# Kernel optimization log

Hardware: AMD Instinct MI355X
Metric: run time of the kernel (lower is better)

## Reference

```python
import jax, jax.numpy as jnp
import numpy as np

DIM = 256
HEADS = 8
HEAD_DIM = DIM // HEADS
EDGE_TYPES = 8  # edge_type_count; table has EDGE_TYPES+1 rows, row 0 is padding
B, N = 2, 2048
EPS = 1e-5


def layer_norm(x, g, b):
    mu = jnp.mean(x, axis=-1, keepdims=True)
    var = jnp.mean(jnp.square(x - mu), axis=-1, keepdims=True)
    return (x - mu) * jax.lax.rsqrt(var + EPS) * g + b


def setup_inputs() -> dict:
    key = jax.random.key(0)
    ks = jax.random.split(key, 12)
    s = 0.02
    x = jax.random.normal(ks[0], (B, N, DIM), dtype=jnp.float32)
    edge_types = jax.random.randint(ks[1], (B, N, N), 0, EDGE_TYPES + 1, dtype=jnp.int32)
    node_mask = jax.random.randint(ks[2], (B, N), 0, 2, dtype=jnp.int32).astype(bool)
    qkv_w = jax.random.normal(ks[3], (DIM, 3 * DIM), dtype=jnp.float32) * s
    qkv_b = jnp.zeros((3 * DIM,), jnp.float32)
    proj_w = jax.random.normal(ks[4], (DIM, DIM), dtype=jnp.float32) * s
    proj_b = jnp.zeros((DIM,), jnp.float32)
    edge_bias_table = jax.random.normal(ks[5], (EDGE_TYPES + 1, HEADS), dtype=jnp.float32) * s
    edge_bias_table = edge_bias_table.at[0].set(0.0)  # padding_idx=0
    ln1_g = jnp.ones((DIM,), jnp.float32); ln1_b = jnp.zeros((DIM,), jnp.float32)
    ln2_g = jnp.ones((DIM,), jnp.float32); ln2_b = jnp.zeros((DIM,), jnp.float32)
    ffn_w1 = jax.random.normal(ks[6], (DIM, 4 * DIM), dtype=jnp.float32) * s
    ffn_b1 = jnp.zeros((4 * DIM,), jnp.float32)
    ffn_w2 = jax.random.normal(ks[7], (4 * DIM, DIM), dtype=jnp.float32) * s
    ffn_b2 = jnp.zeros((DIM,), jnp.float32)
    return dict(x=x, edge_types=edge_types, node_mask=node_mask,
                qkv_w=qkv_w, qkv_b=qkv_b, proj_w=proj_w, proj_b=proj_b,
                edge_bias_table=edge_bias_table, ln1_g=ln1_g, ln1_b=ln1_b,
                ln2_g=ln2_g, ln2_b=ln2_b, ffn_w1=ffn_w1, ffn_b1=ffn_b1,
                ffn_w2=ffn_w2, ffn_b2=ffn_b2)


def reference(x, edge_types, node_mask, qkv_w, qkv_b, proj_w, proj_b,
              edge_bias_table, ln1_g, ln1_b, ln2_g, ln2_b,
              ffn_w1, ffn_b1, ffn_w2, ffn_b2):
    scale = HEAD_DIM ** -0.5
    residual = x
    h = layer_norm(x, ln1_g, ln1_b)
    qkv = h @ qkv_w + qkv_b                         # [B,N,3*DIM]
    qkv = qkv.reshape(B, N, 3, HEADS, HEAD_DIM)
    q, k, v = (qkv[:, :, 0].transpose(0, 2, 1, 3),  # [B,H,N,d]
               qkv[:, :, 1].transpose(0, 2, 1, 3),
               qkv[:, :, 2].transpose(0, 2, 1, 3))
    scores = jnp.einsum('bhnd,bhmd->bhnm', q, k) * scale
    bias = edge_bias_table[edge_types]              # [B,N,N,H]
    scores = scores + bias.transpose(0, 3, 1, 2)    # [B,H,N,N]
    eye = jnp.eye(N, dtype=bool)
    edge_mask = (edge_types != 0) | eye[None]
    node_mask_2d = node_mask[:, None, :] & node_mask[:, :, None]
    attn_mask = edge_mask & node_mask_2d            # [B,N,N]
    scores = jnp.where(attn_mask[:, None], scores, -1e9)
    attn = jax.nn.softmax(scores, axis=-1)
    out = jnp.einsum('bhnm,bhmd->bhnd', attn, v)
    out = out.transpose(0, 2, 1, 3).reshape(B, N, DIM)
    out = (out @ proj_w + proj_b) * node_mask[:, :, None]
    x1 = residual + out
    h2 = layer_norm(x1, ln2_g, ln2_b)
    h2 = jax.nn.gelu(h2 @ ffn_w1 + ffn_b1, approximate=False) @ ffn_w2 + ffn_b2
    h2 = h2 * node_mask[:, :, None]
    return x1 + h2
```

## Files before the change

### kernel.cpp

```cpp
#include <hip/hip_runtime.h>
#include <math.h>

#define DIMM 256
#define HEADS 8
#define NB 2048
#define BB 2
#define ROWS (BB*NB)

typedef __attribute__((ext_vector_type(8))) short bf16x8;
typedef __attribute__((ext_vector_type(4))) float f32x4;

__device__ inline unsigned short f2bf(float f) {
    unsigned int u = __float_as_uint(f);
    u += 0x7FFFu + ((u >> 16) & 1u);
    return (unsigned short)(u >> 16);
}
__device__ inline float bf2f(unsigned short u) {
    return __uint_as_float(((unsigned int)u) << 16);
}

__device__ inline int get_mask(const void* nm, int fmt, int idx) {
    if (fmt) return ((const unsigned char*)nm)[idx] != 0;
    return ((const int*)nm)[idx] != 0;
}

__device__ inline void ln8_body(const float* __restrict__ x, const float* __restrict__ g,
                                const float* __restrict__ bb, unsigned short* __restrict__ o,
                                int row, int lane32) {
    int c0 = lane32 * 8;
    float4 v0 = *(const float4*)&x[(size_t)row * DIMM + c0];
    float4 v1 = *(const float4*)&x[(size_t)row * DIMM + c0 + 4];
    float s  = v0.x + v0.y + v0.z + v0.w + v1.x + v1.y + v1.z + v1.w;
    float s2 = v0.x*v0.x + v0.y*v0.y + v0.z*v0.z + v0.w*v0.w
             + v1.x*v1.x + v1.y*v1.y + v1.z*v1.z + v1.w*v1.w;
#pragma unroll
    for (int off = 16; off >= 1; off >>= 1) {
        s  += __shfl_xor(s,  off);
        s2 += __shfl_xor(s2, off);
    }
    float mean = s * (1.0f / DIMM);
    float var  = s2 * (1.0f / DIMM) - mean * mean;
    float rstd = rsqrtf(var + 1e-5f);
    float4 g0 = *(const float4*)&g[c0],  g1 = *(const float4*)&g[c0 + 4];
    float4 b0 = *(const float4*)&bb[c0], b1 = *(const float4*)&bb[c0 + 4];
    ushort4 u0, u1;
    u0.x = f2bf((v0.x - mean) * rstd * g0.x + b0.x);
    u0.y = f2bf((v0.y - mean) * rstd * g0.y + b0.y);
    u0.z = f2bf((v0.z - mean) * rstd * g0.z + b0.z);
    u0.w = f2bf((v0.w - mean) * rstd * g0.w + b0.w);
    u1.x = f2bf((v1.x - mean) * rstd * g1.x + b1.x);
    u1.y = f2bf((v1.y - mean) * rstd * g1.y + b1.y);
    u1.z = f2bf((v1.z - mean) * rstd * g1.z + b1.z);
    u1.w = f2bf((v1.w - mean) * rstd * g1.w + b1.w);
    *(ushort4*)&o[(size_t)row * DIMM + c0]     = u0;
    *(ushort4*)&o[(size_t)row * DIMM + c0 + 4] = u1;
}

__global__ __launch_bounds__(256) void prep_kernel(
    const float* __restrict__ w0, const float* __restrict__ w1,
    const float* __restrict__ w2, const float* __restrict__ w3,
    unsigned short* __restrict__ o0, unsigned short* __restrict__ o1,
    unsigned short* __restrict__ o2, unsigned short* __restrict__ o3,
    const float* __restrict__ x, const float* __restrict__ ln1_g,
    const float* __restrict__ ln1_b, unsigned short* __restrict__ h_ln,
    const int* __restrict__ etypes, const void* __restrict__ nmask,
    unsigned char* __restrict__ emaskP)
{
    __shared__ float tile[64][65];
    __shared__ int fsh;
    int bid = blockIdx.x, t = threadIdx.x;
    if (bid < 192) {
        const float* src; unsigned short* dst; int K, N, idx;
        if (bid < 48)       { src = w0; dst = o0; K = 256;  N = 768;  idx = bid; }
        else if (bid < 64)  { src = w1; dst = o1; K = 256;  N = 256;  idx = bid - 48; }
        else if (bid < 128) { src = w2; dst = o2; K = 256;  N = 1024; idx = bid - 64; }
        else                { src = w3; dst = o3; K = 1024; N = 256;  idx = bid - 128; }
        int ntiles = N >> 6;
        int k0 = (idx / ntiles) * 64, n0 = (idx % ntiles) * 64;
        int r = t >> 4, c4 = (t & 15) * 4;
#pragma unroll
        for (int i = 0; i < 4; ++i) {
            float4 v = *(const float4*)&src[(size_t)(k0 + r + i * 16) * N + n0 + c4];
            tile[r + i * 16][c4 + 0] = v.x;
            tile[r + i * 16][c4 + 1] = v.y;
            tile[r + i * 16][c4 + 2] = v.z;
            tile[r + i * 16][c4 + 3] = v.w;
        }
        __syncthreads();
#pragma unroll
        for (int i = 0; i < 4; ++i) {
            int n = n0 + r + i * 16;
            ushort4 u;
            u.x = f2bf(tile[c4 + 0][r + i * 16]);
            u.y = f2bf(tile[c4 + 1][r + i * 16]);
            u.z = f2bf(tile[c4 + 2][r + i * 16]);
            u.w = f2bf(tile[c4 + 3][r + i * 16]);
            *(ushort4*)&dst[(size_t)n * K + k0 + c4] = u;
        }
    } else if (bid < 704) {
        int row = (bid - 192) * 8 + (t >> 5);
        ln8_body(x, ln1_g, ln1_b, h_ln, row, t & 31);
    } else {
        if (t == 0) fsh = 0;
        __syncthreads();
        if (((const unsigned char*)nmask)[4 * t + 1] != 0) fsh = 1;
        __syncthreads();
        int fm = fsh;
        int unit = (bid - 704) * 4 + (t >> 6);
        int lane = t & 63, quad = lane >> 4, l15 = lane & 15;
        int b = unit >> 12;
        int qt16 = (unit >> 5) & 127;
        int kt = unit & 31;
        int dw[4];
#pragma unroll
        for (int r = 0; r < 4; ++r) {
            int qr = qt16 * 16 + quad * 4 + r;
            int rowv = get_mask(nmask, fm, b * NB + qr);
            unsigned int pk = 0u;
#pragma unroll
            for (int ct = 0; ct < 4; ++ct) {
                int col = kt * 64 + ct * 16 + l15;
                int et = etypes[(size_t)(b * NB + qr) * NB + col];
                int colv = get_mask(nmask, fm, b * NB + col);
                int valid = rowv && colv && ((et != 0) || (col == qr));
                pk |= (valid ? (unsigned int)(et + 1) : 0u) << (ct * 8);
            }
            dw[r] = (int)pk;
        }
        int4 o = {dw[0], dw[1], dw[2], dw[3]};
        *(int4*)(emaskP + (size_t)unit * 1024 + lane * 16) = o;
    }
}

__global__ __launch_bounds__(256) void gemm_qkv_mfma(
    const unsigned short* __restrict__ A, const unsigned short* __restrict__ Bt,
    const float* __restrict__ bias,
    unsigned short* __restrict__ qkvh, unsigned short* __restrict__ vT)
{
    const int K = 256;
    int t = threadIdx.x, w = t >> 6, l = t & 63;
    int l15 = l & 15, quad = l >> 4;
    int n0 = blockIdx.x * 64;
    int m0 = blockIdx.y * 64;
    const unsigned short* ap = A + (size_t)(m0 + w * 16 + l15) * K + quad * 8;
    const unsigned short* bp = Bt + (size_t)(n0 + l15) * K + quad * 8;

    f32x4 acc[4];
#pragma unroll
    for (int c = 0; c < 4; ++c) acc[c] = (f32x4){0.f, 0.f, 0.f, 0.f};

    bf16x8 aA, bA[4], aB, bB[4];
    auto ld = [&](bf16x8& af, bf16x8 (&bf)[4], int k0) {
        af = *(const bf16x8*)(ap + k0);
#pragma unroll
        for (int c = 0; c < 4; ++c)
            bf[c] = *(const bf16x8*)(bp + (size_t)(c * 16) * K + k0);
    };
    auto pr = [&](const bf16x8& af, const bf16x8 (&bf)[4]) {
#pragma unroll
        for (int c = 0; c < 4; ++c)
            acc[c] = __builtin_amdgcn_mfma_f32_16x16x32_bf16(af, bf[c], acc[c], 0, 0, 0);
    };
    ld(aA, bA, 0);
    for (int k0 = 0; k0 < K; k0 += 64) {
        ld(aB, bB, k0 + 32);
        pr(aA, bA);
        if (k0 + 64 < K) ld(aA, bA, k0 + 64);
        pr(aB, bB);
    }

    if (n0 < 512) {
#pragma unroll
        for (int r = 0; r < 4; ++r) {
            int row = m0 + w * 16 + quad * 4 + r;
#pragma unroll
            for (int c = 0; c < 4; ++c) {
                int col = n0 + c * 16 + l15;
                qkvh[(size_t)row * 512 + col] = f2bf(acc[c][r] + bias[col]);
            }
        }
    } else {
        int bb_ = m0 >> 11;
        int n = (m0 + w * 16 + quad * 4) & 2047;
#pragma unroll
        for (int c = 0; c < 4; ++c) {
            int col = n0 + c * 16 + l15 - 512;
            int hidx = col >> 5, d = col & 31;
            float bs = bias[n0 + c * 16 + l15];
            ushort4 u;
            u.x = f2bf(acc[c][0] + bs);
            u.y = f2bf(acc[c][1] + bs);
            u.z = f2bf(acc[c][2] + bs);
            u.w = f2bf(acc[c][3] + bs);
            *(ushort4*)&vT[(size_t)((bb_ * HEADS + hidx) * 32 + d) * NB + n] = u;
        }
    }
}

__global__ __launch_bounds__(256) void attn_mfma(
    const unsigned short* __restrict__ qkvh,
    const unsigned short* __restrict__ vT,
    const unsigned char* __restrict__ emaskP,
    const float* __restrict__ table,
    unsigned short* __restrict__ OpH, float* __restrict__ lpart)
{
    __shared__ unsigned short P[4][16][72];
    __shared__ float tab2m[16];

    int t = threadIdx.x;
    int w = t >> 6, l = t & 63;
    int l15 = l & 15, quad = l >> 4;
    int h = blockIdx.y;
    int z = blockIdx.z, b = z >> 2, sp = z & 3;
    int q0 = blockIdx.x * 64 + w * 16;
    int kbase = sp * (NB / 4);

    if (t < 16) tab2m[t] = (t >= 1 && t < 10) ? __expf(table[(t - 1) * 8 + h]) : 0.f;
    __syncthreads();

    const float scale = 0.17677669529663689f;

    bf16x8 aq = *(const bf16x8*)(qkvh + (size_t)(b * NB + q0 + l15) * 512 + h * 32 + quad * 8);

    const unsigned short* kp = qkvh + (size_t)(b * NB + l15) * 512 + 256 + h * 32 + quad * 8;
    const unsigned short* vp = vT + (size_t)((b * HEADS + h) * 32 + l15) * NB + quad * 8;
    int qt16 = blockIdx.x * 4 + w;
    const unsigned char* ep = emaskP + (size_t)((b * 128 + qt16) * 32) * 1024 + l * 16;

    float lacc[4] = {0.f, 0.f, 0.f, 0.f};
    f32x4 O0 = {0.f, 0.f, 0.f, 0.f}, O1 = {0.f, 0.f, 0.f, 0.f};

    auto loadtile = [&](bf16x8 (&kf)[4], bf16x8 (&vf)[2][2], int4& ef, int m0) {
#pragma unroll
        for (int ct = 0; ct < 4; ++ct)
            kf[ct] = *(const bf16x8*)(kp + (size_t)(m0 + ct * 16) * 512);
#pragma unroll
        for (int ks = 0; ks < 2; ++ks) {
            vf[ks][0] = *(const bf16x8*)(vp + m0 + ks * 32);
            vf[ks][1] = *(const bf16x8*)(vp + 16 * NB + m0 + ks * 32);
        }
        ef = *(const int4*)(ep + (size_t)(m0 >> 6) * 1024);
    };

    auto process = [&](const bf16x8 (&kf)[4], const bf16x8 (&vf)[2][2], const int4& ef) {
        unsigned int ew[4] = {(unsigned int)ef.x, (unsigned int)ef.y,
                              (unsigned int)ef.z, (unsigned int)ef.w};
#pragma unroll
        for (int ct = 0; ct < 4; ++ct) {
            f32x4 zero = {0.f, 0.f, 0.f, 0.f};
            f32x4 s = __builtin_amdgcn_mfma_f32_16x16x32_bf16(aq, kf[ct], zero, 0, 0, 0);
#pragma unroll
            for (int r = 0; r < 4; ++r) {
                unsigned int c = (ew[r] >> (ct * 8)) & 0xffu;
                float p = __expf(s[r] * scale) * tab2m[c];
                lacc[r] += p;
                P[w][quad * 4 + r][ct * 16 + l15] = f2bf(p);
            }
        }
#pragma unroll
        for (int ks = 0; ks < 2; ++ks) {
            bf16x8 pa = *(const bf16x8*)&P[w][l15][ks * 32 + quad * 8];
            O0 = __builtin_amdgcn_mfma_f32_16x16x32_bf16(pa, vf[ks][0], O0, 0, 0, 0);
            O1 = __builtin_amdgcn_mfma_f32_16x16x32_bf16(pa, vf[ks][1], O1, 0, 0, 0);
        }
    };

    bf16x8 kA[4], kB[4];
    bf16x8 vA[2][2], vB[2][2];
    int4 eA, eB;

    loadtile(kA, vA, eA, kbase);
    for (int m0 = kbase; m0 < kbase + NB / 4; m0 += 128) {
        loadtile(kB, vB, eB, m0 + 64);
        process(kA, vA, eA);
        if (m0 + 128 < kbase + NB / 4) loadtile(kA, vA, eA, m0 + 128);
        process(kB, vB, eB);
    }

    unsigned short* Ob = OpH + (size_t)sp * ROWS * DIMM;
#pragma unroll
    for (int r = 0; r < 4; ++r) {
        float s = lacc[r];
        s += __shfl_xor(s, 1); s += __shfl_xor(s, 2);
        s += __shfl_xor(s, 4); s += __shfl_xor(s, 8);
        int row = b * NB + q0 + quad * 4 + r;
        Ob[(size_t)row * DIMM + h * 32 + l15]      = f2bf(O0[r]);
        Ob[(size_t)row * DIMM + h * 32 + 16 + l15] = f2bf(O1[r]);
        if (l15 == 0) lpart[(size_t)sp * ROWS * 8 + (size_t)row * 8 + h] = s;
    }
}

__global__ __launch_bounds__(1024) void megaback(
    const unsigned short* __restrict__ OpH, const float* __restrict__ lpart,
    const unsigned short* __restrict__ projT, const float* __restrict__ proj_b,
    const float* __restrict__ x, const void* __restrict__ nmask,
    const float* __restrict__ g2, const float* __restrict__ b2,
    const unsigned short* __restrict__ f1T, const float* __restrict__ ffn_b1,
    const unsigned short* __restrict__ f2T, const float* __restrict__ ffn_b2,
    float* __restrict__ out)
{
    __shared__ float rinv_l[16][8];
    __shared__ float stats[16][2];
    __shared__ float redn[16][16][2];
    __shared__ unsigned short Astage[16][264];
    __shared__ float x1s[16][260];
    __shared__ unsigned short hstage[16][264];
    __shared__ unsigned short midstage[16][1032];
    __shared__ int fsh;

    int t = threadIdx.x;
    int w = t >> 6, l = t & 63;
    int l15 = l & 15, quad = l >> 4;
    int grow0 = blockIdx.x * 16;

    if (t == 0) fsh = 0;
    __syncthreads();
    if (((const unsigned char*)nmask)[4 * t + 1] != 0) fsh = 1;

    if (t < 128) {
        int row = t >> 3, h = t & 7;
        float s = 0.f;
#pragma unroll
        for (int sp = 0; sp < 4; ++sp)
            s += lpart[(size_t)sp * ROWS * 8 + (size_t)(grow0 + row) * 8 + h];
        rinv_l[row][h] = (s > 0.f) ? 1.f / s : 0.f;
    }
    __syncthreads();
    int fm = fsh;

    {
        int row = t >> 6, col4 = (t & 63) * 4;
        float rinv = rinv_l[row][col4 >> 5];
        float o0 = 0.f, o1 = 0.f, o2 = 0.f, o3 = 0.f;
#pragma unroll
        for (int sp = 0; sp < 4; ++sp) {
            ushort4 u = *(const ushort4*)&OpH[(size_t)sp * ROWS * DIMM +
                                             (size_t)(grow0 + row) * DIMM + col4];
            o0 += bf2f(u.x); o1 += bf2f(u.y); o2 += bf2f(u.z); o3 += bf2f(u.w);
        }
        ushort4 u;
        u.x = f2bf(o0 * rinv); u.y = f2bf(o1 * rinv);
        u.z = f2bf(o2 * rinv); u.w = f2bf(o3 * rinv);
        *(ushort4*)&Astage[row][col4] = u;
    }
    __syncthreads();

    {
        int col = w * 16 + l15;
        f32x4 acc = (f32x4){0.f, 0.f, 0.f, 0.f};
        const unsigned short* bp = projT + (size_t)col * 256 + quad * 8;
        bf16x8 sb[4];
#pragma unroll
        for (int i = 0; i < 4; ++i) sb[i] = *(const bf16x8*)(bp + i * 32);
#pragma unroll
        for (int ch = 0; ch < 8; ++ch) {
            bf16x8 a = *(const bf16x8*)&Astage[l15][ch * 32 + quad * 8];
            acc = __builtin_amdgcn_mfma_f32_16x16x32_bf16(a, sb[ch & 3], acc, 0, 0, 0);
            if (ch + 4 < 8) sb[ch & 3] = *(const bf16x8*)(bp + (ch + 4) * 32);
        }
        float bs = proj_b[col];
#pragma unroll
        for (int r = 0; r < 4; ++r) {
            int row = quad * 4 + r, grow = grow0 + row;
            float mk = (float)get_mask(nmask, fm, grow);
            float v = (acc[r] + bs) * mk + x[(size_t)grow * DIMM + col];
            x1s[row][col] = v;
            float s = v, s2 = v * v;
#pragma unroll
            for (int off = 1; off < 16; off <<= 1) {
                s += __shfl_xor(s, off); s2 += __shfl_xor(s2, off);
            }
            if (l15 == 0) { redn[row][w][0] = s; redn[row][w][1] = s2; }
        }
    }
    __syncthreads();
    if (t < 16) {
        float s = 0.f, s2 = 0.f;
#pragma unroll
        for (int ww = 0; ww < 16; ++ww) { s += redn[t][ww][0]; s2 += redn[t][ww][1]; }
        float mean = s * (1.f / DIMM);
        float var  = s2 * (1.f / DIMM) - mean * mean;
        stats[t][0] = mean; stats[t][1] = rsqrtf(var + 1e-5f);
    }
    __syncthreads();

    {
        int col = w * 16 + l15;
        float gv = g2[col], bv = b2[col];
#pragma unroll
        for (int r = 0; r < 4; ++r) {
            int row = quad * 4 + r;
            float hv = (x1s[row][col] - stats[row][0]) * stats[row][1] * gv + bv;
            hstage[row][col] = f2bf(hv);
        }
    }
    __syncthreads();

    {
        f32x4 acc[4];
#pragma unroll
        for (int c = 0; c < 4; ++c) acc[c] = (f32x4){0.f, 0.f, 0.f, 0.f};
        const unsigned short* bp = f1T + (size_t)(w * 64 + l15) * 256 + quad * 8;
        bf16x8 bA[4], bB[4];
#pragma unroll
        for (int c = 0; c < 4; ++c) bA[c] = *(const bf16x8*)(bp + (size_t)(c * 16) * 256);
#pragma unroll
        for (int ch = 0; ch < 8; ++ch) {
            bf16x8 a = *(const bf16x8*)&hstage[l15][ch * 32 + quad * 8];
            if (ch + 1 < 8) {
#pragma unroll
                for (int c = 0; c < 4; ++c)
                    bB[c] = *(const bf16x8*)(bp + (size_t)(c * 16) * 256 + (ch + 1) * 32);
            }
#pragma unroll
            for (int c = 0; c < 4; ++c)
                acc[c] = __builtin_amdgcn_mfma_f32_16x16x32_bf16(a, bA[c], acc[c], 0, 0, 0);
#pragma unroll
            for (int c = 0; c < 4; ++c) bA[c] = bB[c];
        }
#pragma unroll
        for (int c = 0; c < 4; ++c) {
            int col = w * 64 + c * 16 + l15;
            float bs = ffn_b1[col];
#pragma unroll
            for (int r = 0; r < 4; ++r) {
                float v = acc[c][r] + bs;
                float x2 = v * v;
                float p = v * fmaf(0.07135481f, x2, 1.5957691f);
                float e = __expf(p);
                float gl = v * (e / (e + 1.f));
                midstage[quad * 4 + r][col] = f2bf(gl);
            }
        }
    }
    __syncthreads();

    {
        int col = w * 16 + l15;
        f32x4 acc = (f32x4){0.f, 0.f, 0.f, 0.f};
        const unsigned short* bp = f2T + (size_t)col * 1024 + quad * 8;
        bf16x8 sb[4];
#pragma unroll
        for (int i = 0; i < 4; ++i) sb[i] = *(const bf16x8*)(bp + i * 32);
#pragma unroll
        for (int ch = 0; ch < 32; ++ch) {
            bf16x8 a = *(const bf16x8*)&midstage[l15][ch * 32 + quad * 8];
            acc = __builtin_amdgcn_mfma_f32_16x16x32_bf16(a, sb[ch & 3], acc, 0, 0, 0);
            if (ch + 4 < 32) sb[ch & 3] = *(const bf16x8*)(bp + (ch + 4) * 32);
        }
        float bs = ffn_b2[col];
#pragma unroll
        for (int r = 0; r < 4; ++r) {
            int row = quad * 4 + r, grow = grow0 + row;
            float mk = (float)get_mask(nmask, fm, grow);
            out[(size_t)grow * DIMM + col] = x1s[row][col] + (acc[r] + bs) * mk;
        }
    }
}

extern "C" void kernel_launch(void* const* d_in, const int* in_sizes, int n_in,
                              void* d_out, int out_size, void* d_ws, size_t ws_size,
                              hipStream_t stream) {
    const float* x       = (const float*)d_in[0];
    const int*   etypes  = (const int*)d_in[1];
    const void*  nmask   = d_in[2];
    const float* qkv_w   = (const float*)d_in[3];
    const float* qkv_b   = (const float*)d_in[4];
    const float* proj_w  = (const float*)d_in[5];
    const float* proj_b  = (const float*)d_in[6];
    const float* table   = (const float*)d_in[7];
    const float* ln1_g   = (const float*)d_in[8];
    const float* ln1_b   = (const float*)d_in[9];
    const float* ln2_g   = (const float*)d_in[10];
    const float* ln2_b   = (const float*)d_in[11];
    const float* ffn_w1  = (const float*)d_in[12];
    const float* ffn_b1  = (const float*)d_in[13];
    const float* ffn_w2  = (const float*)d_in[14];
    const float* ffn_b2  = (const float*)d_in[15];
    float* out = (float*)d_out;
    float* ws  = (float*)d_ws;

    float* lpart = ws;
    unsigned short* ub = (unsigned short*)(ws + 131072);
    unsigned short* h_ln   = ub;
    unsigned short* qkvh   = ub + 1048576;
    unsigned short* vT     = ub + 3145728;
    unsigned short* OpH    = ub + 4194304;
    unsigned short* qkvT   = ub + 8388608;
    unsigned short* projT  = ub + 8585216;
    unsigned short* f1T    = ub + 8650752;
    unsigned short* f2T    = ub + 8912896;
    unsigned char* emaskP  = (unsigned char*)(ub + 9175040);

    prep_kernel<<<dim3(2752), dim3(256), 0, stream>>>(
        qkv_w, proj_w, ffn_w1, ffn_w2, qkvT, projT, f1T, f2T,
        x, ln1_g, ln1_b, h_ln, etypes, nmask, emaskP);
    gemm_qkv_mfma<<<dim3(12, 64), dim3(256), 0, stream>>>(h_ln, qkvT, qkv_b, qkvh, vT);
    attn_mfma<<<dim3(NB/64, HEADS, BB*4), dim3(256), 0, stream>>>(
        qkvh, vT, emaskP, table, OpH, lpart);
    megaback<<<dim3(ROWS/16), dim3(1024), 0, stream>>>(
        OpH, lpart, projT, proj_b, x, nmask, ln2_g, ln2_b,
        f1T, ffn_b1, f2T, ffn_b2, out);
}
```

Measured before the change: 233.1 us.

## Compute transposed attention scores so P feeds PV MFMA from registers

The attention kernel now computes S^T = K·Q^T, so each lane holds four consecutive key columns for one query row. The probabilities can then be packed straight into a bf16x4 operand for the 16x16x16 MFMA against V, with no LDS round trip through the shared P buffer. The softmax scale is folded into Q in the QKV GEMM epilogue. The edge-mask packing kernel is rearranged to match the new column order and now uses vectorized int4 loads of edge types and node masks. The trade-off is more MFMA instructions of a smaller shape, plus bf16 rounding of Q after scaling.

```diff
diff --git a/kernel.cpp b/kernel.cpp
--- a/kernel.cpp
+++ b/kernel.cpp
@@ -8,6 +8,7 @@
 #define ROWS (BB*NB)
 
 typedef __attribute__((ext_vector_type(8))) short bf16x8;
+typedef __attribute__((ext_vector_type(4))) short bf16x4;
 typedef __attribute__((ext_vector_type(4))) float f32x4;
 
 __device__ inline unsigned short f2bf(float f) {
@@ -111,21 +112,32 @@
         int b = unit >> 12;
         int qt16 = (unit >> 5) & 127;
         int kt = unit & 31;
+        int qr = qt16 * 16 + l15;
+        int rowv = get_mask(nmask, fm, b * NB + qr);
+        const int* erow = etypes + (size_t)(b * NB + qr) * NB;
         int dw[4];
 #pragma unroll
-        for (int r = 0; r < 4; ++r) {
-            int qr = qt16 * 16 + quad * 4 + r;
-            int rowv = get_mask(nmask, fm, b * NB + qr);
+        for (int t16 = 0; t16 < 4; ++t16) {
+            int col0 = kt * 64 + t16 * 16 + quad * 4;
+            int4 e4 = *(const int4*)(erow + col0);
+            int ee[4] = {e4.x, e4.y, e4.z, e4.w};
+            int cv[4];
+            if (fm) {
+                unsigned int m4 = *(const unsigned int*)((const unsigned char*)nmask + b * NB + col0);
+                cv[0] = (m4 & 0xffu) != 0;     cv[1] = (m4 & 0xff00u) != 0;
+                cv[2] = (m4 & 0xff0000u) != 0; cv[3] = (m4 >> 24) != 0;
+            } else {
+                int4 m4 = *(const int4*)((const int*)nmask + b * NB + col0);
+                cv[0] = m4.x != 0; cv[1] = m4.y != 0; cv[2] = m4.z != 0; cv[3] = m4.w != 0;
+            }
             unsigned int pk = 0u;
 #pragma unroll
-            for (int ct = 0; ct < 4; ++ct) {
-                int col = kt * 64 + ct * 16 + l15;
-                int et = etypes[(size_t)(b * NB + qr) * NB + col];
-                int colv = get_mask(nmask, fm, b * NB + col);
-                int valid = rowv && colv && ((et != 0) || (col == qr));
-                pk |= (valid ? (unsigned int)(et + 1) : 0u) << (ct * 8);
+            for (int r = 0; r < 4; ++r) {
+                int col = col0 + r;
+                int valid = rowv && cv[r] && ((ee[r] != 0) || (col == qr));
+                pk |= (valid ? (unsigned int)(ee[r] + 1) : 0u) << (r * 8);
             }
-            dw[r] = (int)pk;
+            dw[t16] = (int)pk;
         }
         int4 o = {dw[0], dw[1], dw[2], dw[3]};
         *(int4*)(emaskP + (size_t)unit * 1024 + lane * 16) = o;
@@ -170,13 +182,14 @@
     }
 
     if (n0 < 512) {
+        float sc = (n0 < 256) ? 0.17677669529663689f : 1.0f;
 #pragma unroll
         for (int r = 0; r < 4; ++r) {
             int row = m0 + w * 16 + quad * 4 + r;
 #pragma unroll
             for (int c = 0; c < 4; ++c) {
                 int col = n0 + c * 16 + l15;
-                qkvh[(size_t)row * 512 + col] = f2bf(acc[c][r] + bias[col]);
+                qkvh[(size_t)row * 512 + col] = f2bf((acc[c][r] + bias[col]) * sc);
             }
         }
     } else {
@@ -204,7 +217,6 @@
     const float* __restrict__ table,
     unsigned short* __restrict__ OpH, float* __restrict__ lpart)
 {
-    __shared__ unsigned short P[4][16][72];
     __shared__ float tab2m[16];
 
     int t = threadIdx.x;
@@ -213,81 +225,75 @@
     int h = blockIdx.y;
     int z = blockIdx.z, b = z >> 2, sp = z & 3;
     int q0 = blockIdx.x * 64 + w * 16;
-    int kbase = sp * (NB / 4);
+    int kbase = sp * (NB / 4), kend = kbase + NB / 4;
 
     if (t < 16) tab2m[t] = (t >= 1 && t < 10) ? __expf(table[(t - 1) * 8 + h]) : 0.f;
     __syncthreads();
 
-    const float scale = 0.17677669529663689f;
-
-    bf16x8 aq = *(const bf16x8*)(qkvh + (size_t)(b * NB + q0 + l15) * 512 + h * 32 + quad * 8);
-
-    const unsigned short* kp = qkvh + (size_t)(b * NB + l15) * 512 + 256 + h * 32 + quad * 8;
-    const unsigned short* vp = vT + (size_t)((b * HEADS + h) * 32 + l15) * NB + quad * 8;
+    bf16x8 bq = *(const bf16x8*)(qkvh + (size_t)(b * NB + q0 + l15) * 512 + h * 32 + quad * 8);
+
+    const unsigned short* kp  = qkvh + (size_t)(b * NB + l15) * 512 + 256 + h * 32 + quad * 8;
+    const unsigned short* vp0 = vT + (size_t)((b * HEADS + h) * 32 + l15) * NB + quad * 4;
+    const unsigned short* vp1 = vp0 + (size_t)16 * NB;
     int qt16 = blockIdx.x * 4 + w;
     const unsigned char* ep = emaskP + (size_t)((b * 128 + qt16) * 32) * 1024 + l * 16;
 
-    float lacc[4] = {0.f, 0.f, 0.f, 0.f};
+    float lacc = 0.f;
     f32x4 O0 = {0.f, 0.f, 0.f, 0.f}, O1 = {0.f, 0.f, 0.f, 0.f};
 
-    auto loadtile = [&](bf16x8 (&kf)[4], bf16x8 (&vf)[2][2], int4& ef, int m0) {
-#pragma unroll
-        for (int ct = 0; ct < 4; ++ct)
-            kf[ct] = *(const bf16x8*)(kp + (size_t)(m0 + ct * 16) * 512);
-#pragma unroll
-        for (int ks = 0; ks < 2; ++ks) {
-            vf[ks][0] = *(const bf16x8*)(vp + m0 + ks * 32);
-            vf[ks][1] = *(const bf16x8*)(vp + 16 * NB + m0 + ks * 32);
+    bf16x8 kA[4], kB[4];
+    bf16x4 vA[4][2], vB[4][2];
+    int4 eA, eB;
+
+    auto loadtile = [&](bf16x8 (&kf)[4], bf16x4 (&vf)[4][2], int4& ef, int m0) {
+#pragma unroll
+        for (int t16 = 0; t16 < 4; ++t16) {
+            kf[t16]    = *(const bf16x8*)(kp + (size_t)(m0 + t16 * 16) * 512);
+            vf[t16][0] = *(const bf16x4*)(vp0 + m0 + t16 * 16);
+            vf[t16][1] = *(const bf16x4*)(vp1 + m0 + t16 * 16);
         }
         ef = *(const int4*)(ep + (size_t)(m0 >> 6) * 1024);
     };
 
-    auto process = [&](const bf16x8 (&kf)[4], const bf16x8 (&vf)[2][2], const int4& ef) {
-        unsigned int ew[4] = {(unsigned int)ef.x, (unsigned int)ef.y,
-                              (unsigned int)ef.z, (unsigned int)ef.w};
-#pragma unroll
-        for (int ct = 0; ct < 4; ++ct) {
+    auto process = [&](const bf16x8 (&kf)[4], const bf16x4 (&vf)[4][2], const int4& ef) {
+        int ew[4] = {ef.x, ef.y, ef.z, ef.w};
+#pragma unroll
+        for (int t16 = 0; t16 < 4; ++t16) {
             f32x4 zero = {0.f, 0.f, 0.f, 0.f};
-            f32x4 s = __builtin_amdgcn_mfma_f32_16x16x32_bf16(aq, kf[ct], zero, 0, 0, 0);
-#pragma unroll
-            for (int r = 0; r < 4; ++r) {
-                unsigned int c = (ew[r] >> (ct * 8)) & 0xffu;
-                float p = __expf(s[r] * scale) * tab2m[c];
-                lacc[r] += p;
-                P[w][quad * 4 + r][ct * 16 + l15] = f2bf(p);
-            }
-        }
-#pragma unroll
-        for (int ks = 0; ks < 2; ++ks) {
-            bf16x8 pa = *(const bf16x8*)&P[w][l15][ks * 32 + quad * 8];
-            O0 = __builtin_amdgcn_mfma_f32_16x16x32_bf16(pa, vf[ks][0], O0, 0, 0, 0);
-            O1 = __builtin_amdgcn_mfma_f32_16x16x32_bf16(pa, vf[ks][1], O1, 0, 0, 0);
+            f32x4 sT = __builtin_amdgcn_mfma_f32_16x16x32_bf16(kf[t16], bq, zero, 0, 0, 0);
+            unsigned int e = (unsigned int)ew[t16];
+            float p0 = __expf(sT[0]) * tab2m[e & 0xffu];
+            float p1 = __expf(sT[1]) * tab2m[(e >> 8) & 0xffu];
+            float p2 = __expf(sT[2]) * tab2m[(e >> 16) & 0xffu];
+            float p3 = __expf(sT[3]) * tab2m[e >> 24];
+            lacc += (p0 + p1) + (p2 + p3);
+            bf16x4 pb;
+            pb[0] = (short)f2bf(p0); pb[1] = (short)f2bf(p1);
+            pb[2] = (short)f2bf(p2); pb[3] = (short)f2bf(p3);
+            O0 = __builtin_amdgcn_mfma_f32_16x16x16bf16_1k(vf[t16][0], pb, O0, 0, 0, 0);
+            O1 = __builtin_amdgcn_mfma_f32_16x16x16bf16_1k(vf[t16][1], pb, O1, 0, 0, 0);
         }
     };
 
-    bf16x8 kA[4], kB[4];
-    bf16x8 vA[2][2], vB[2][2];
-    int4 eA, eB;
-
     loadtile(kA, vA, eA, kbase);
-    for (int m0 = kbase; m0 < kbase + NB / 4; m0 += 128) {
+    for (int m0 = kbase; m0 < kend; m0 += 128) {
         loadtile(kB, vB, eB, m0 + 64);
         process(kA, vA, eA);
-        if (m0 + 128 < kbase + NB / 4) loadtile(kA, vA, eA, m0 + 128);
+        if (m0 + 128 < kend) loadtile(kA, vA, eA, m0 + 128);
         process(kB, vB, eB);
     }
 
+    lacc += __shfl_xor(lacc, 16);
+    lacc += __shfl_xor(lacc, 32);
+
     unsigned short* Ob = OpH + (size_t)sp * ROWS * DIMM;
-#pragma unroll
-    for (int r = 0; r < 4; ++r) {
-        float s = lacc[r];
-        s += __shfl_xor(s, 1); s += __shfl_xor(s, 2);
-        s += __shfl_xor(s, 4); s += __shfl_xor(s, 8);
-        int row = b * NB + q0 + quad * 4 + r;
-        Ob[(size_t)row * DIMM + h * 32 + l15]      = f2bf(O0[r]);
-        Ob[(size_t)row * DIMM + h * 32 + 16 + l15] = f2bf(O1[r]);
-        if (l15 == 0) lpart[(size_t)sp * ROWS * 8 + (size_t)row * 8 + h] = s;
-    }
+    int row = b * NB + q0 + l15;
+    ushort4 u0, u1;
+    u0.x = f2bf(O0[0]); u0.y = f2bf(O0[1]); u0.z = f2bf(O0[2]); u0.w = f2bf(O0[3]);
+    u1.x = f2bf(O1[0]); u1.y = f2bf(O1[1]); u1.z = f2bf(O1[2]); u1.w = f2bf(O1[3]);
+    *(ushort4*)&Ob[(size_t)row * DIMM + h * 32 + quad * 4]      = u0;
+    *(ushort4*)&Ob[(size_t)row * DIMM + h * 32 + 16 + quad * 4] = u1;
+    if (quad == 0) lpart[(size_t)sp * ROWS * 8 + (size_t)row * 8 + h] = lacc;
 }
 
 __global__ __launch_bounds__(1024) void megaback(
```

Result: slower. 255.8 us (+9.7%).
